# Optimization experiments

Hardware: AMD Instinct MI355X
Metric: run time of the kernel (lower is better)

The kernel has to match this reference:

```python
import jax, jax.numpy as jnp
import numpy as np

EMBED_DIM = 1024
NUM_HEADS = 16
HEAD_DIM = EMBED_DIM // NUM_HEADS


def setup_inputs() -> dict:
    key = jax.random.key(0)
    k1, k2, k3 = jax.random.split(key, 3)
    scale = 1.0 / np.sqrt(EMBED_DIM)
    x = jax.random.normal(k1, (2, 2048, EMBED_DIM), dtype=jnp.float32)
    w_qkv = jax.random.normal(k2, (EMBED_DIM, 3 * EMBED_DIM), dtype=jnp.float32) * scale
    b_qkv = jnp.zeros((3 * EMBED_DIM,), dtype=jnp.float32)
    w_out = jax.random.normal(k3, (EMBED_DIM, EMBED_DIM), dtype=jnp.float32) * scale
    b_out = jnp.zeros((EMBED_DIM,), dtype=jnp.float32)
    return {"x": x, "w_qkv": w_qkv, "b_qkv": b_qkv, "w_out": w_out, "b_out": b_out}


def reference(x, w_qkv, b_qkv, w_out, b_out):
    B, N, C = x.shape
    H, D = NUM_HEADS, HEAD_DIM
    qkv = x @ w_qkv + b_qkv                      # [B, N, 3C]
    qkv = qkv.reshape(B, N, 3, H, D)
    q = qkv[:, :, 0].transpose(0, 2, 1, 3)       # [B, H, N, D]
    k = qkv[:, :, 1].transpose(0, 2, 1, 3)
    v = qkv[:, :, 2].transpose(0, 2, 1, 3)
    scores = jnp.einsum('bhnd,bhmd->bhnm', q, k) / jnp.sqrt(jnp.float32(D))
    attn = jax.nn.softmax(scores, axis=-1)
    out = jnp.einsum('bhnm,bhmd->bhnd', attn, v)  # [B, H, N, D]
    out = out.transpose(0, 2, 1, 3).reshape(B, N, C)
    return out @ w_out + b_out
```

## Files before the change

kernel.cpp:

```cpp
#include <hip/hip_runtime.h>
#include <stdint.h>

typedef unsigned short u16;
typedef short s16x8 __attribute__((ext_vector_type(8)));
typedef unsigned short u16x8 __attribute__((ext_vector_type(8)));
typedef unsigned short u16x4 __attribute__((ext_vector_type(4)));
typedef float f32x4 __attribute__((ext_vector_type(4)));
typedef float f32x16 __attribute__((ext_vector_type(16)));
typedef unsigned int u32x2 __attribute__((ext_vector_type(2)));
typedef unsigned int u32x4 __attribute__((ext_vector_type(4)));

#if __has_builtin(__builtin_amdgcn_exp2f)
#define EXP2F(x) __builtin_amdgcn_exp2f(x)
#else
#define EXP2F(x) exp2f(x)
#endif

#define QSCALE 0.18033688011112042f

__device__ __forceinline__ u16 f2b(float f) {
  union { float f; uint32_t u; } v; v.f = f;
  uint32_t r = (v.u + 0x7fffu + ((v.u >> 16) & 1u)) >> 16;
  return (u16)r;
}

__device__ __forceinline__ uint32_t pkhi(uint32_t hi, uint32_t lo) {
#if __has_builtin(__builtin_amdgcn_perm)
  return __builtin_amdgcn_perm(hi, lo, 0x07060302u);
#else
  return (lo >> 16) | (hi & 0xffff0000u);
#endif
}

__device__ __forceinline__ void plswap(uint32_t& a, uint32_t& b) {
#if __has_builtin(__builtin_amdgcn_permlane32_swap)
  typedef unsigned int uv2 __attribute__((ext_vector_type(2)));
  uv2 r = __builtin_amdgcn_permlane32_swap(a, b, false, false);
  a = r[0];
  b = r[1];
#else
  asm volatile("v_permlane32_swap_b32 %0, %1" : "+v"(a), "+v"(b));
#endif
}

__device__ __forceinline__ void sync_lds() {
  asm volatile("s_waitcnt lgkmcnt(0)\ns_barrier" ::: "memory");
}

__device__ __forceinline__ void gld16(const void* g, void* l) {
  __builtin_amdgcn_global_load_lds((__attribute__((address_space(1))) void*)g,
                                   (__attribute__((address_space(3))) void*)l,
                                   16, 0, 0);
}

__global__ __launch_bounds__(256)
void prep(const float* __restrict__ x, u16* __restrict__ xb,
          const float* __restrict__ w_qkv, u16* __restrict__ wqT,
          const float* __restrict__ w_out, u16* __restrict__ woT) {
  __shared__ float tile[32][33];
  const int bid = blockIdx.x;
  const int t = threadIdx.x;
  if (bid < 2048) {
    const size_t i = ((size_t)bid * 256 + t) * 8;
    f32x4 v0 = *(const f32x4*)(x + i);
    f32x4 v1 = *(const f32x4*)(x + i + 4);
    u16x8 u;
#pragma unroll
    for (int j = 0; j < 4; j++) { u[j] = f2b(v0[j]); u[4 + j] = f2b(v1[j]); }
    *(u16x8*)(xb + i) = u;
    return;
  }
  const float* src;
  u16* dst;
  int N, nb, kb;
  if (bid < 5120) {
    const int b2 = bid - 2048;
    src = w_qkv; dst = wqT; N = 3072;
    nb = (b2 % 96) * 32; kb = (b2 / 96) * 32;
  } else {
    const int b3 = bid - 5120;
    src = w_out; dst = woT; N = 1024;
    nb = (b3 & 31) * 32; kb = (b3 >> 5) * 32;
  }
  const int tx = t & 31, ty = t >> 5;
#pragma unroll
  for (int i = 0; i < 4; i++)
    tile[ty + i * 8][tx] = src[(size_t)(kb + ty + i * 8) * N + nb + tx];
  __syncthreads();
#pragma unroll
  for (int i = 0; i < 4; i++)
    dst[(size_t)(nb + ty + i * 8) * 1024 + kb + tx] = f2b(tile[tx][ty + i * 8]);
}

template <int EPI, int WN>
__global__ __launch_bounds__(256, 3)
void gemm_bt(const u16* __restrict__ A, const u16* __restrict__ Bt,
             const float* __restrict__ bias, float* __restrict__ outF,
             u16* __restrict__ outQ, u16* __restrict__ outK,
             u16* __restrict__ outVt, int M, int N, int K) {
  constexpr int BN = WN * 64;
  constexpr int RW = 4 / WN;
  constexpr int MI = 128 / RW / 16;
  constexpr int NBI = WN * 2;
  constexpr int SMEM = (EPI == 0) ? 34816 : (16384 + WN * 8192);
  __shared__ char smem[SMEM];
  u16* As = (u16*)smem;
  u16* Bs = As + 128 * 64;

  const int t = threadIdx.x;
  const int m0 = blockIdx.y * 128, n0 = blockIdx.x * BN;
  const int w = t >> 6, lane = t & 63;
  const int wm = w / WN, wn = w % WN;
  const int quad = lane >> 4, lrow = lane & 15;
  const int r8 = lane >> 3, s8 = lane & 7;
  const int csw = (s8 ^ r8) * 8;

  const u16* gA = A + (size_t)(m0 + w * 32 + r8) * K + csw;
  const u16* gB = Bt + (size_t)(n0 + w * (WN * 16) + r8) * K + csw;
  u16* wAs = As + (w * 32 + r8) * 64 + s8 * 8;
  u16* wBs = Bs + (w * (WN * 16) + r8) * 64 + s8 * 8;

  f32x4 acc[MI][4];
#pragma unroll
  for (int i = 0; i < MI; i++)
#pragma unroll
    for (int j = 0; j < 4; j++) {
      f32x4 z = {0.f, 0.f, 0.f, 0.f};
      acc[i][j] = z;
    }

  u16x8 pa[4], pb[NBI];
#pragma unroll
  for (int i = 0; i < 4; i++) pa[i] = *(const u16x8*)(gA + (size_t)(i * 8) * K);
#pragma unroll
  for (int i = 0; i < NBI; i++) pb[i] = *(const u16x8*)(gB + (size_t)(i * 8) * K);

  const int KT = K >> 6;
  for (int kt = 0; kt < KT; ++kt) {
    sync_lds();
#pragma unroll
    for (int i = 0; i < 4; i++) *(u16x8*)(wAs + i * 8 * 64) = pa[i];
#pragma unroll
    for (int i = 0; i < NBI; i++) *(u16x8*)(wBs + i * 8 * 64) = pb[i];
    if (kt + 1 < KT) {
      const size_t off = (size_t)(kt + 1) * 64;
#pragma unroll
      for (int i = 0; i < 4; i++)
        pa[i] = *(const u16x8*)(gA + (size_t)(i * 8) * K + off);
#pragma unroll
      for (int i = 0; i < NBI; i++)
        pb[i] = *(const u16x8*)(gB + (size_t)(i * 8) * K + off);
    }
    sync_lds();

#pragma unroll
    for (int ks = 0; ks < 2; ks++) {
      s16x8 a[MI], b[4];
#pragma unroll
      for (int i = 0; i < MI; i++)
        a[i] = *(const s16x8*)&As[(wm * (MI * 16) + i * 16 + lrow) * 64 +
                                  (((ks * 4 + quad) ^ (lrow & 7)) * 8)];
#pragma unroll
      for (int j = 0; j < 4; j++)
        b[j] = *(const s16x8*)&Bs[(wn * 64 + j * 16 + lrow) * 64 +
                                  (((ks * 4 + quad) ^ (lrow & 7)) * 8)];
#pragma unroll
      for (int i = 0; i < MI; i++)
#pragma unroll
        for (int j = 0; j < 4; j++)
          acc[i][j] = __builtin_amdgcn_mfma_f32_16x16x32_bf16(a[i], b[j],
                                                              acc[i][j], 0, 0, 0);
    }
  }

  if (EPI == 1) {
#pragma unroll
    for (int i = 0; i < MI; i++) {
      const int row = m0 + wm * (MI * 16) + i * 16 + quad * 4;
#pragma unroll
      for (int j = 0; j < 4; j++) {
        const int col = n0 + wn * 64 + j * 16 + lrow;
        const float bv = bias[col];
#pragma unroll
        for (int r = 0; r < 4; r++)
          outF[(size_t)(row + r) * N + col] = acc[i][j][r] + bv;
      }
    }
    return;
  }

  sync_lds();
  u16* rp = (u16*)smem + w * (64 * 68);
  const int cb = n0 + wn * 64;
  const int which = cb >> 10;
  const int h = (cb & 1023) >> 6;
  const int rbase = m0 + wm * 64;
  const int bb = rbase >> 11, nn0 = rbase & 2047;
  const int rl = lane >> 3, cc = (lane & 7) * 8;

  if (which != 2) {
    const float s = (which == 0) ? QSCALE : 1.0f;
#pragma unroll
    for (int i = 0; i < 4; i++)
#pragma unroll
      for (int j = 0; j < 4; j++) {
        const float bv = bias[cb + j * 16 + lrow];
#pragma unroll
        for (int r = 0; r < 4; r++)
          rp[(i * 16 + quad * 4 + r) * 68 + j * 16 + lrow] =
              f2b((acc[i][j][r] + bv) * s);
      }
    u16* dst = ((which == 0) ? outQ : outK) +
               ((size_t)(bb * 16 + h) * 2048 + nn0) * 64;
#pragma unroll
    for (int it = 0; it < 8; it++) {
      const int row = it * 8 + rl;
      *(u16x8*)&dst[(size_t)row * 64 + cc] = *(const u16x8*)&rp[row * 68 + cc];
    }
  } else {
#pragma unroll
    for (int i = 0; i < 4; i++)
#pragma unroll
      for (int j = 0; j < 4; j++) {
        const float bv = bias[cb + j * 16 + lrow];
        u16x4 pk;
#pragma unroll
        for (int r = 0; r < 4; r++) pk[r] = f2b(acc[i][j][r] + bv);
        *(u16x4*)&rp[(j * 16 + lrow) * 68 + i * 16 + quad * 4] = pk;
      }
    u16* dst = outVt + ((size_t)(bb * 16 + h) * 64) * 2048 + nn0;
#pragma unroll
    for (int it = 0; it < 8; it++) {
      const int d = it * 8 + rl;
      *(u16x8*)&dst[(size_t)d * 2048 + cc] = *(const u16x8*)&rp[d * 68 + cc];
    }
  }
}

__global__ __launch_bounds__(512, 4)
void attn_kernel(const u16* __restrict__ Q, const u16* __restrict__ Kg,
                 const u16* __restrict__ Vt, u16* __restrict__ AO) {
  __shared__ u16 Ks[2][2][64 * 64];
  __shared__ u16 Vs[2][2][64 * 64];
  __shared__ float Lsh[4][32];

  const int t = threadIdx.x;
  const int bh = blockIdx.x;
  const int qt = blockIdx.y;
  const int w = t >> 6, lane = t & 63;
  const int kh = w >> 2, wi = w & 3;
  const int l31 = lane & 31, lh = lane >> 5;
  const int srow8 = lane >> 3, chunk = lane & 7;
  const int csw = chunk ^ srow8;
  const size_t base = (size_t)bh * 2048 * 64;

  s16x8 qf[4];
  {
    const u16* qp = Q + base + (size_t)(qt * 128 + wi * 32 + l31) * 64 + lh * 8;
#pragma unroll
    for (int ks = 0; ks < 4; ks++) qf[ks] = *(const s16x8*)(qp + ks * 16);
  }

  int cx[4];
#pragma unroll
  for (int ks = 0; ks < 4; ks++) cx[ks] = ((2 * ks + lh) ^ (l31 & 7)) * 8;

  const u16* kgl = Kg + base + (size_t)(kh * 1024 + wi * 16 + srow8) * 64 +
                   csw * 8;
  const u16* vgl = Vt + base + (size_t)(wi * 16 + srow8) * 2048 + kh * 1024 +
                   csw * 8;
  const int lbase = (wi * 16) * 64;

  const short one_bf16 = 0x3F80;
  s16x8 ones = {one_bf16, one_bf16, one_bf16, one_bf16,
                one_bf16, one_bf16, one_bf16, one_bf16};

  f32x16 ot0, ot1, liacc;
#pragma unroll
  for (int e = 0; e < 16; e++) { ot0[e] = 0.f; ot1[e] = 0.f; liacc[e] = 0.f; }

  gld16(kgl, &Ks[kh][0][lbase]);
  gld16(kgl + 512, &Ks[kh][0][lbase + 512]);
  gld16(vgl, &Vs[kh][0][lbase]);
  gld16(vgl + (size_t)8 * 2048, &Vs[kh][0][lbase + 512]);

  for (int kt = 0; kt < 16; kt++) {
    const int cur = kt & 1;
    __syncthreads();
    if (kt + 1 < 16) {
      const int nxt = cur ^ 1;
      gld16(kgl + (size_t)(kt + 1) * 4096, &Ks[kh][nxt][lbase]);
      gld16(kgl + (size_t)(kt + 1) * 4096 + 512, &Ks[kh][nxt][lbase + 512]);
      gld16(vgl + (kt + 1) * 64, &Vs[kh][nxt][lbase]);
      gld16(vgl + (kt + 1) * 64 + (size_t)8 * 2048, &Vs[kh][nxt][lbase + 512]);
    }

    f32x16 sc0, sc1;
#pragma unroll
    for (int e = 0; e < 16; e++) { sc0[e] = 0.f; sc1[e] = 0.f; }
#pragma unroll
    for (int ks = 0; ks < 4; ks++) {
      s16x8 k0 = *(const s16x8*)&Ks[kh][cur][l31 * 64 + cx[ks]];
      s16x8 k1 = *(const s16x8*)&Ks[kh][cur][(32 + l31) * 64 + cx[ks]];
      sc0 = __builtin_amdgcn_mfma_f32_32x32x16_bf16(k0, qf[ks], sc0, 0, 0, 0);
      sc1 = __builtin_amdgcn_mfma_f32_32x32x16_bf16(k1, qf[ks], sc1, 0, 0, 0);
    }

    uint32_t P[2][4][2];
#pragma unroll
    for (int tb = 0; tb < 2; tb++) {
      const f32x16& s = tb ? sc1 : sc0;
#pragma unroll
      for (int g = 0; g < 4; g++) {
        uint32_t u[4];
#pragma unroll
        for (int r = 0; r < 4; r++)
          u[r] = __builtin_bit_cast(uint32_t, EXP2F(s[g * 4 + r]));
        P[tb][g][0] = pkhi(u[1], u[0]);
        P[tb][g][1] = pkhi(u[3], u[2]);
      }
    }

#pragma unroll
    for (int tb = 0; tb < 2; tb++) {
#pragma unroll
      for (int gp = 0; gp < 2; gp++) {
        uint32_t w0 = P[tb][2 * gp][0], w2 = P[tb][2 * gp + 1][0];
        uint32_t w1 = P[tb][2 * gp][1], w3 = P[tb][2 * gp + 1][1];
        plswap(w0, w2);
        plswap(w1, w3);
        u32x4 fw = {w0, w1, w2, w3};
        s16x8 pf = __builtin_bit_cast(s16x8, fw);
        const int ks = tb * 2 + gp;
        s16x8 v0 = *(const s16x8*)&Vs[kh][cur][l31 * 64 + cx[ks]];
        s16x8 v1 = *(const s16x8*)&Vs[kh][cur][(32 + l31) * 64 + cx[ks]];
        ot0 = __builtin_amdgcn_mfma_f32_32x32x16_bf16(v0, pf, ot0, 0, 0, 0);
        ot1 = __builtin_amdgcn_mfma_f32_32x32x16_bf16(v1, pf, ot1, 0, 0, 0);
        liacc = __builtin_amdgcn_mfma_f32_32x32x16_bf16(ones, pf, liacc, 0, 0, 0);
      }
    }
  }

  float* Osm = (float*)Ks;
  const float lihalf = liacc[0];
  __syncthreads();
  if (kh == 1) {
#pragma unroll
    for (int e = 0; e < 16; e++) {
      Osm[((wi * 2 + 0) * 16 + e) * 64 + lane] = ot0[e];
      Osm[((wi * 2 + 1) * 16 + e) * 64 + lane] = ot1[e];
    }
    if (lh == 0) Lsh[wi][l31] = lihalf;
  }
  __syncthreads();
  if (kh == 0) {
    const float inv = 1.0f / (lihalf + Lsh[wi][l31]);
    const int bb = bh >> 4, h = bh & 15;
    const int qn = qt * 128 + wi * 32 + l31;
    u16* dst = AO + (size_t)(bb * 2048 + qn) * 1024 + h * 64;
#pragma unroll
    for (int dt = 0; dt < 2; dt++) {
      const f32x16& o = dt ? ot1 : ot0;
#pragma unroll
      for (int g = 0; g < 4; g++) {
        u16x4 pk;
#pragma unroll
        for (int r = 0; r < 4; r++) {
          const float v =
              o[g * 4 + r] + Osm[((wi * 2 + dt) * 16 + g * 4 + r) * 64 + lane];
          pk[r] = f2b(v * inv);
        }
        *(u16x4*)&dst[dt * 32 + g * 8 + lh * 4] = pk;
      }
    }
  }
}

extern "C" void kernel_launch(void* const* d_in, const int* in_sizes, int n_in,
                              void* d_out, int out_size, void* d_ws,
                              size_t ws_size, hipStream_t stream) {
  const float* x     = (const float*)d_in[0];
  const float* w_qkv = (const float*)d_in[1];
  const float* b_qkv = (const float*)d_in[2];
  const float* w_out = (const float*)d_in[3];
  const float* b_out = (const float*)d_in[4];
  float* out = (float*)d_out;

  char* ws = (char*)d_ws;
  u16* wqT = (u16*)ws; ws += (size_t)3072 * 1024 * 2;
  u16* woT = (u16*)ws; ws += (size_t)1024 * 1024 * 2;
  u16* q   = (u16*)ws; ws += (size_t)32 * 2048 * 64 * 2;
  u16* k   = (u16*)ws; ws += (size_t)32 * 2048 * 64 * 2;
  u16* vt  = (u16*)ws; ws += (size_t)32 * 64 * 2048 * 2;
  u16* xb  = (u16*)ws; ws += (size_t)4096 * 1024 * 2;
  u16* ao  = xb;

  prep<<<dim3(6144), 256, 0, stream>>>(x, xb, w_qkv, wqT, w_out, woT);
  gemm_bt<0, 2><<<dim3(24, 32), 256, 0, stream>>>(xb, wqT, b_qkv, nullptr, q, k,
                                                  vt, 4096, 3072, 1024);
  attn_kernel<<<dim3(32, 16), 512, 0, stream>>>(q, k, vt, ao);
  gemm_bt<1, 1><<<dim3(16, 32), 256, 0, stream>>>(ao, woT, b_out, out, nullptr,
                                                  nullptr, nullptr, 4096, 1024, 1024);
}
```

Before: 173.1 us.

## Double-buffer GEMM LDS tiles with direct global-to-LDS loads

The bf16 GEMM main loop used to stage each next K-tile through registers and then copy it into a single LDS buffer, which needed two barriers per iteration. It now uses two LDS buffers and fills the next tile with global_load_lds (direct global-to-LDS DMA) while MFMAs run on the current one, so only one barrier per iteration remains. The launch-bounds occupancy hint is dropped. The larger LDS footprint (two buffers) may reduce how many blocks fit per CU.

```diff
diff --git a/kernel.cpp b/kernel.cpp
--- a/kernel.cpp
+++ b/kernel.cpp
@@ -41,10 +41,6 @@
 #else
   asm volatile("v_permlane32_swap_b32 %0, %1" : "+v"(a), "+v"(b));
 #endif
-}
-
-__device__ __forceinline__ void sync_lds() {
-  asm volatile("s_waitcnt lgkmcnt(0)\ns_barrier" ::: "memory");
 }
 
 __device__ __forceinline__ void gld16(const void* g, void* l) {
@@ -93,7 +89,7 @@
 }
 
 template <int EPI, int WN>
-__global__ __launch_bounds__(256, 3)
+__global__ __launch_bounds__(256)
 void gemm_bt(const u16* __restrict__ A, const u16* __restrict__ Bt,
              const float* __restrict__ bias, float* __restrict__ outF,
              u16* __restrict__ outQ, u16* __restrict__ outK,
@@ -101,11 +97,10 @@
   constexpr int BN = WN * 64;
   constexpr int RW = 4 / WN;
   constexpr int MI = 128 / RW / 16;
-  constexpr int NBI = WN * 2;
-  constexpr int SMEM = (EPI == 0) ? 34816 : (16384 + WN * 8192);
-  __shared__ char smem[SMEM];
-  u16* As = (u16*)smem;
-  u16* Bs = As + 128 * 64;
+  constexpr int ABUF = 128 * 64;
+  constexpr int BBUF = BN * 64;
+  constexpr int BUF = ABUF + BBUF;
+  __shared__ u16 smem[2 * BUF];
 
   const int t = threadIdx.x;
   const int m0 = blockIdx.y * 128, n0 = blockIdx.x * BN;
@@ -117,8 +112,6 @@
 
   const u16* gA = A + (size_t)(m0 + w * 32 + r8) * K + csw;
   const u16* gB = Bt + (size_t)(n0 + w * (WN * 16) + r8) * K + csw;
-  u16* wAs = As + (w * 32 + r8) * 64 + s8 * 8;
-  u16* wBs = Bs + (w * (WN * 16) + r8) * 64 + s8 * 8;
 
   f32x4 acc[MI][4];
 #pragma unroll
@@ -129,30 +122,36 @@
       acc[i][j] = z;
     }
 
-  u16x8 pa[4], pb[NBI];
-#pragma unroll
-  for (int i = 0; i < 4; i++) pa[i] = *(const u16x8*)(gA + (size_t)(i * 8) * K);
-#pragma unroll
-  for (int i = 0; i < NBI; i++) pb[i] = *(const u16x8*)(gB + (size_t)(i * 8) * K);
+  {
+    u16* As = smem;
+    u16* Bs = smem + ABUF;
+#pragma unroll
+    for (int i = 0; i < 4; i++)
+      gld16(gA + (size_t)(i * 8) * K, &As[(w * 32 + i * 8) * 64]);
+#pragma unroll
+    for (int i = 0; i < 2 * WN; i++)
+      gld16(gB + (size_t)(i * 8) * K, &Bs[(w * (WN * 16) + i * 8) * 64]);
+  }
 
   const int KT = K >> 6;
   for (int kt = 0; kt < KT; ++kt) {
-    sync_lds();
-#pragma unroll
-    for (int i = 0; i < 4; i++) *(u16x8*)(wAs + i * 8 * 64) = pa[i];
-#pragma unroll
-    for (int i = 0; i < NBI; i++) *(u16x8*)(wBs + i * 8 * 64) = pb[i];
+    const int cur = kt & 1;
+    __syncthreads();
     if (kt + 1 < KT) {
-      const size_t off = (size_t)(kt + 1) * 64;
+      u16* As = smem + (cur ^ 1) * BUF;
+      u16* Bs = As + ABUF;
+      const u16* a = gA + (size_t)(kt + 1) * 64;
+      const u16* b = gB + (size_t)(kt + 1) * 64;
 #pragma unroll
       for (int i = 0; i < 4; i++)
-        pa[i] = *(const u16x8*)(gA + (size_t)(i * 8) * K + off);
-#pragma unroll
-      for (int i = 0; i < NBI; i++)
-        pb[i] = *(const u16x8*)(gB + (size_t)(i * 8) * K + off);
-    }
-    sync_lds();
-
+        gld16(a + (size_t)(i * 8) * K, &As[(w * 32 + i * 8) * 64]);
+#pragma unroll
+      for (int i = 0; i < 2 * WN; i++)
+        gld16(b + (size_t)(i * 8) * K, &Bs[(w * (WN * 16) + i * 8) * 64]);
+    }
+
+    const u16* As = smem + cur * BUF;
+    const u16* Bs = As + ABUF;
 #pragma unroll
     for (int ks = 0; ks < 2; ks++) {
       s16x8 a[MI], b[4];
@@ -189,8 +188,8 @@
     return;
   }
 
-  sync_lds();
-  u16* rp = (u16*)smem + w * (64 * 68);
+  __syncthreads();
+  u16* rp = smem + w * (64 * 68);
   const int cb = n0 + wn * 64;
   const int which = cb >> 10;
   const int h = (cb & 1023) >> 6;
```

After: 173.2 us. Within noise of the previous version (+0.1%).
